# Optimization experiments

Hardware: AMD Instinct MI355X
Metric: run time of the kernel (lower is better)

## Reference

```python
import jax, jax.numpy as jnp
import numpy as np


def _fake_quant(x, bits, axis):
    """AQT-style abs-max symmetric fake quantization.

    IntNumerics(bits, preserve_zero=True, preserve_max_val=True, clip=True,
    round=True) with AbsMaxCalibration: bound = 2^(bits-1)-1,
    scale = absmax/bound (stop-gradient), q = round(clip(x/scale)),
    dequant = q*scale. Round uses straight-through estimator.
    """
    bound = float(2 ** (bits - 1) - 1)
    absmax = jax.lax.stop_gradient(
        jnp.max(jnp.abs(x), axis=axis, keepdims=True))
    scale = absmax / bound
    scale = jnp.where(scale == 0.0, jnp.ones_like(scale), scale)
    s = x / scale
    clipped = jnp.clip(s, -bound, bound)  # clip_gradient=True semantics
    rounded = clipped + jax.lax.stop_gradient(jnp.round(clipped) - clipped)
    return rounded * scale


def setup_inputs() -> dict:
    key = jax.random.key(0)
    k1, k2, k3 = jax.random.split(key, 3)
    B, S, D, F = 4, 2048, 4096, 4096
    x = jax.random.normal(k1, (B, S, D), dtype=jnp.float32)
    # lecun_normal over (in, out)
    kernel = jax.random.normal(k2, (D, F), dtype=jnp.float32) / np.sqrt(D)
    bias = jax.random.normal(k3, (F,), dtype=jnp.float32) * 0.01
    return {"x": x, "kernel": kernel, "bias": bias}


def reference(x, kernel, bias):
    # int8 fake-quant of activations: abs-max over contracting (last) axis
    xq = _fake_quant(x, bits=8, axis=-1)
    # int8 fake-quant of kernel: abs-max over contracting axis (0) -> per out-col
    kq = _fake_quant(kernel, bits=8, axis=0)
    # quantized dot_general: contract last axis of x with axis 0 of kernel
    y = jnp.einsum('bsd,df->bsf', xq, kq)
    # int16 fake-quant of bias (calibration_axes=-1 over the whole vector)
    bq16 = _fake_quant(bias, bits=16, axis=-1)
    y = y + bq16[None, None, :]
    # int8 output requant, per-row abs-max over feature axis
    out = _fake_quant(y, bits=8, axis=-1)
    return out
```

## Files before the change

### kernel.cpp

```cpp
#include <hip/hip_runtime.h>
#include <stdint.h>

typedef int int32x4 __attribute__((ext_vector_type(4)));

#define M_ROWS 8192
#define K_DIM  4096
#define N_DIM  4096

#define GPTR(p) ((const __attribute__((address_space(1))) unsigned int*)(p))
#define LPTR(p) ((__attribute__((address_space(3))) unsigned int*)(p))

__device__ __forceinline__ float block_absmax_256(float v, float* red) {
#pragma unroll
  for (int off = 32; off > 0; off >>= 1)
    v = fmaxf(v, __shfl_down(v, off, 64));
  const int w = threadIdx.x >> 6;
  if ((threadIdx.x & 63) == 0) red[w] = v;
  __syncthreads();
  return fmaxf(fmaxf(red[0], red[1]), fmaxf(red[2], red[3]));
}

__global__ void quant_x_kernel(const float* __restrict__ x,
                               int8_t* __restrict__ qx,
                               float* __restrict__ sx) {
  __shared__ float red[4];
  const int row = blockIdx.x;
  const int t = threadIdx.x;
  const float* xr = x + (size_t)row * K_DIM;
  float4 v[4];
  float m = 0.0f;
#pragma unroll
  for (int i = 0; i < 4; ++i) {
    v[i] = *(const float4*)(xr + t * 16 + i * 4);
    m = fmaxf(m, fmaxf(fmaxf(fabsf(v[i].x), fabsf(v[i].y)),
                       fmaxf(fabsf(v[i].z), fabsf(v[i].w))));
  }
  float amax = block_absmax_256(m, red);
  float scale = amax / 127.0f;
  if (scale == 0.0f) scale = 1.0f;
  if (t == 0) sx[row] = scale;
  int words[4];
#pragma unroll
  for (int i = 0; i < 4; ++i) {
    float a = fminf(fmaxf(v[i].x / scale, -127.0f), 127.0f);
    float b = fminf(fmaxf(v[i].y / scale, -127.0f), 127.0f);
    float c = fminf(fmaxf(v[i].z / scale, -127.0f), 127.0f);
    float d = fminf(fmaxf(v[i].w / scale, -127.0f), 127.0f);
    int qa = (int)rintf(a), qb = (int)rintf(b), qc = (int)rintf(c), qd = (int)rintf(d);
    words[i] = (qa & 255) | ((qb & 255) << 8) | ((qc & 255) << 16) | ((qd & 255) << 24);
  }
  *(int4*)(qx + (size_t)row * K_DIM + t * 16) =
      make_int4(words[0], words[1], words[2], words[3]);
}

__global__ void colmax_kernel(const float* __restrict__ k,
                              unsigned int* __restrict__ cm) {
  const int c = blockIdx.x * 256 + threadIdx.x;
  const int r0 = blockIdx.y * 128;
  float m = 0.0f;
  for (int i = 0; i < 128; ++i)
    m = fmaxf(m, fabsf(k[(size_t)(r0 + i) * N_DIM + c]));
  atomicMax(&cm[c], __float_as_uint(m));
}

__global__ void finalize_kernel(const float* __restrict__ cm,
                                float* __restrict__ sk,
                                const float* __restrict__ bias,
                                float* __restrict__ bq) {
  __shared__ float red[4];
  const int t = threadIdx.x;
  if (blockIdx.x < 16) {
    const int c = blockIdx.x * 256 + t;
    float s = cm[c] / 127.0f;
    if (s == 0.0f) s = 1.0f;
    sk[c] = s;
  } else {
    float4 v[4];
    float m = 0.0f;
#pragma unroll
    for (int i = 0; i < 4; ++i) {
      v[i] = *(const float4*)(bias + t * 16 + i * 4);
      m = fmaxf(m, fmaxf(fmaxf(fabsf(v[i].x), fabsf(v[i].y)),
                         fmaxf(fabsf(v[i].z), fabsf(v[i].w))));
    }
    float amax = block_absmax_256(m, red);
    float s = amax / 32767.0f;
    if (s == 0.0f) s = 1.0f;
#pragma unroll
    for (int i = 0; i < 4; ++i) {
      float4 o;
      o.x = rintf(fminf(fmaxf(v[i].x / s, -32767.0f), 32767.0f)) * s;
      o.y = rintf(fminf(fmaxf(v[i].y / s, -32767.0f), 32767.0f)) * s;
      o.z = rintf(fminf(fmaxf(v[i].z / s, -32767.0f), 32767.0f)) * s;
      o.w = rintf(fminf(fmaxf(v[i].w / s, -32767.0f), 32767.0f)) * s;
      *(float4*)(bq + t * 16 + i * 4) = o;
    }
  }
}

__global__ void quant_kT_kernel(const float* __restrict__ kern,
                                const float* __restrict__ cm,
                                int8_t* __restrict__ qkT) {
  __shared__ int8_t tile[64][68];
  const int t = threadIdx.x;
  const int c0 = blockIdx.x * 64;
  const int r0 = blockIdx.y * 64;
  const int tc = t & 63;
  const int tr = t >> 6;
  float s = cm[c0 + tc] / 127.0f;
  if (s == 0.0f) s = 1.0f;
#pragma unroll
  for (int i = 0; i < 16; ++i) {
    const int r = r0 + tr + i * 4;
    float u = kern[(size_t)r * N_DIM + c0 + tc] / s;
    u = fminf(fmaxf(u, -127.0f), 127.0f);
    tile[tc][tr + i * 4] = (int8_t)rintf(u);
  }
  __syncthreads();
  const int cl = t >> 2;
  const int ch = (t & 3) * 16;
  int w4[4];
#pragma unroll
  for (int j = 0; j < 4; ++j) w4[j] = *(const int*)&tile[cl][ch + j * 4];
  *(int4*)(qkT + (size_t)(c0 + cl) * K_DIM + r0 + ch) =
      make_int4(w4[0], w4[1], w4[2], w4[3]);
}

#define BM 128
#define BN 128
#define BK 64

__global__ void gemm_kernel(const int8_t* __restrict__ qx,
                            const int8_t* __restrict__ qkT,
                            const float* __restrict__ sx,
                            const float* __restrict__ sk,
                            const float* __restrict__ bq,
                            float* __restrict__ out) {
  __shared__ int32x4 AsV[512];
  __shared__ int32x4 BsV[512];
  char* As = (char*)AsV;
  char* Bs = (char*)BsV;

  const int t = threadIdx.x;
  const int w = t >> 6;
  const int l = t & 63;
  const int wm = w >> 1, wn = w & 1;
  const int rowBase = blockIdx.y * BM;
  const int colBase = blockIdx.x * BN;

  const int sw = (l & 3) ^ ((l >> 2) & 3) ^ (l >> 4);

  const int8_t* gA = qx  + (size_t)(rowBase + (l >> 2)) * K_DIM + sw * 16;
  const int8_t* gB = qkT + (size_t)(colBase + (l >> 2)) * K_DIM + sw * 16;

  int aoff[4], boff[4];
#pragma unroll
  for (int mt = 0; mt < 4; ++mt)
    aoff[mt] = (wm * 64 + mt * 16 + (l & 15)) * 64 + sw * 16;
#pragma unroll
  for (int nt = 0; nt < 4; ++nt)
    boff[nt] = (wn * 64 + nt * 16 + (l & 15)) * 64 + sw * 16;

  int32x4 zero = {0, 0, 0, 0};
  int32x4 acc[4][4];
#pragma unroll
  for (int mt = 0; mt < 4; ++mt)
#pragma unroll
    for (int nt = 0; nt < 4; ++nt) acc[mt][nt] = zero;

  for (int k0 = 0; k0 < K_DIM; k0 += BK) {
    __syncthreads();
#pragma unroll
    for (int j = 0; j < 2; ++j) {
      const int chunk = j * 4 + w;
      __builtin_amdgcn_global_load_lds(
          GPTR(gA + (size_t)chunk * 16 * K_DIM + k0),
          LPTR(As + chunk * 1024), 16, 0, 0);
      __builtin_amdgcn_global_load_lds(
          GPTR(gB + (size_t)chunk * 16 * K_DIM + k0),
          LPTR(Bs + chunk * 1024), 16, 0, 0);
    }
    __syncthreads();

    int32x4 af[4], bf[4];
#pragma unroll
    for (int mt = 0; mt < 4; ++mt) af[mt] = *(const int32x4*)(As + aoff[mt]);
#pragma unroll
    for (int nt = 0; nt < 4; ++nt) bf[nt] = *(const int32x4*)(Bs + boff[nt]);
#pragma unroll
    for (int mt = 0; mt < 4; ++mt)
#pragma unroll
      for (int nt = 0; nt < 4; ++nt)
        acc[mt][nt] = __builtin_amdgcn_mfma_i32_16x16x64_i8(
            af[mt], bf[nt], acc[mt][nt], 0, 0, 0);
  }

  const int lr = (l >> 4) * 4;
  const int lc = l & 15;
#pragma unroll
  for (int mt = 0; mt < 4; ++mt) {
    const int r0 = rowBase + wm * 64 + mt * 16 + lr;
    float sxr[4];
#pragma unroll
    for (int r = 0; r < 4; ++r) sxr[r] = sx[r0 + r];
#pragma unroll
    for (int nt = 0; nt < 4; ++nt) {
      const int c = colBase + wn * 64 + nt * 16 + lc;
      const float skc = sk[c];
      const float bqc = bq[c];
#pragma unroll
      for (int r = 0; r < 4; ++r)
        out[(size_t)(r0 + r) * N_DIM + c] =
            (float)acc[mt][nt][r] * (sxr[r] * skc) + bqc;
    }
  }
}

__global__ void requant_kernel(float* __restrict__ y) {
  __shared__ float red[4];
  const int row = blockIdx.x;
  const int t = threadIdx.x;
  float* yr = y + (size_t)row * N_DIM;
  float4 v[4];
  float m = 0.0f;
#pragma unroll
  for (int i = 0; i < 4; ++i) {
    v[i] = *(const float4*)(yr + i * 1024 + t * 4);
    m = fmaxf(m, fmaxf(fmaxf(fabsf(v[i].x), fabsf(v[i].y)),
                       fmaxf(fabsf(v[i].z), fabsf(v[i].w))));
  }
  float amax = block_absmax_256(m, red);
  float s = amax / 127.0f;
  if (s == 0.0f) s = 1.0f;
#pragma unroll
  for (int i = 0; i < 4; ++i) {
    float4 o;
    o.x = rintf(fminf(fmaxf(v[i].x / s, -127.0f), 127.0f)) * s;
    o.y = rintf(fminf(fmaxf(v[i].y / s, -127.0f), 127.0f)) * s;
    o.z = rintf(fminf(fmaxf(v[i].z / s, -127.0f), 127.0f)) * s;
    o.w = rintf(fminf(fmaxf(v[i].w / s, -127.0f), 127.0f)) * s;
    *(float4*)(yr + i * 1024 + t * 4) = o;
  }
}

extern "C" void kernel_launch(void* const* d_in, const int* in_sizes, int n_in,
                              void* d_out, int out_size, void* d_ws, size_t ws_size,
                              hipStream_t stream) {
  (void)in_sizes; (void)n_in; (void)out_size; (void)ws_size;
  const float* x    = (const float*)d_in[0];
  const float* kern = (const float*)d_in[1];
  const float* bias = (const float*)d_in[2];
  float* out = (float*)d_out;

  char* w8 = (char*)d_ws;
  int8_t* qx  = (int8_t*)w8;
  int8_t* qkT = (int8_t*)(w8 + 33554432);
  float* sx   = (float*)(w8 + 50331648);
  float* cm   = (float*)(w8 + 50331648 + 32768);
  float* sk   = (float*)(w8 + 50331648 + 49152);
  float* bq   = (float*)(w8 + 50331648 + 65536);

  hipMemsetAsync(cm, 0, 4096 * sizeof(float), stream);
  quant_x_kernel<<<M_ROWS, 256, 0, stream>>>(x, qx, sx);
  colmax_kernel<<<dim3(16, 32), 256, 0, stream>>>(kern, (unsigned int*)cm);
  finalize_kernel<<<17, 256, 0, stream>>>(cm, sk, bias, bq);
  quant_kT_kernel<<<dim3(64, 64), 256, 0, stream>>>(kern, cm, qkT);
  gemm_kernel<<<dim3(N_DIM / BN, M_ROWS / BM), 256, 0, stream>>>(qx, qkT, sx, sk, bq, out);
  requant_kernel<<<M_ROWS, 256, 0, stream>>>(out);
}
```

Baseline: 503.6 us.

## Double GEMM K-tile to 128 with new LDS swizzle and vectorize kernel quant

The GEMM K-step doubles from 64 to 128. Each iteration now loads twice as much A and B into LDS, using a new 8-row-per-chunk XOR swizzle, and runs two MFMA sub-steps. This halves the number of barrier pairs and loop iterations per output tile, at the cost of double the LDS use, which may reduce occupancy. The kernel-transpose quantizer now reads float4 vectors and writes int4 rows from a padded tile, cutting the number of global load instructions.

```diff
diff --git a/kernel.cpp b/kernel.cpp
--- a/kernel.cpp
+++ b/kernel.cpp
@@ -101,34 +101,37 @@
 __global__ void quant_kT_kernel(const float* __restrict__ kern,
                                 const float* __restrict__ cm,
                                 int8_t* __restrict__ qkT) {
-  __shared__ int8_t tile[64][68];
+  __shared__ int8_t tile[64][80];
   const int t = threadIdx.x;
   const int c0 = blockIdx.x * 64;
   const int r0 = blockIdx.y * 64;
-  const int tc = t & 63;
-  const int tr = t >> 6;
-  float s = cm[c0 + tc] / 127.0f;
-  if (s == 0.0f) s = 1.0f;
-#pragma unroll
-  for (int i = 0; i < 16; ++i) {
-    const int r = r0 + tr + i * 4;
-    float u = kern[(size_t)r * N_DIM + c0 + tc] / s;
-    u = fminf(fmaxf(u, -127.0f), 127.0f);
-    tile[tc][tr + i * 4] = (int8_t)rintf(u);
+  const int colg = (t & 15) * 4;
+  const int row = t >> 4;
+  float s[4];
+#pragma unroll
+  for (int j = 0; j < 4; ++j) {
+    float v = cm[c0 + colg + j] / 127.0f;
+    s[j] = (v == 0.0f) ? 1.0f : v;
+  }
+#pragma unroll
+  for (int i = 0; i < 4; ++i) {
+    const int r = row + i * 16;
+    float4 v = *(const float4*)&kern[(size_t)(r0 + r) * N_DIM + c0 + colg];
+    tile[colg + 0][r] = (int8_t)rintf(fminf(fmaxf(v.x / s[0], -127.0f), 127.0f));
+    tile[colg + 1][r] = (int8_t)rintf(fminf(fmaxf(v.y / s[1], -127.0f), 127.0f));
+    tile[colg + 2][r] = (int8_t)rintf(fminf(fmaxf(v.z / s[2], -127.0f), 127.0f));
+    tile[colg + 3][r] = (int8_t)rintf(fminf(fmaxf(v.w / s[3], -127.0f), 127.0f));
   }
   __syncthreads();
-  const int cl = t >> 2;
-  const int ch = (t & 3) * 16;
-  int w4[4];
-#pragma unroll
-  for (int j = 0; j < 4; ++j) w4[j] = *(const int*)&tile[cl][ch + j * 4];
-  *(int4*)(qkT + (size_t)(c0 + cl) * K_DIM + r0 + ch) =
-      make_int4(w4[0], w4[1], w4[2], w4[3]);
+  const int f = t >> 2;
+  const int seg = (t & 3) * 16;
+  int4 w = *(const int4*)&tile[f][seg];
+  *(int4*)(qkT + (size_t)(c0 + f) * K_DIM + r0 + seg) = w;
 }
 
 #define BM 128
 #define BN 128
-#define BK 64
+#define BK 128
 
 __global__ void gemm_kernel(const int8_t* __restrict__ qx,
                             const int8_t* __restrict__ qkT,
@@ -136,8 +139,8 @@
                             const float* __restrict__ sk,
                             const float* __restrict__ bq,
                             float* __restrict__ out) {
-  __shared__ int32x4 AsV[512];
-  __shared__ int32x4 BsV[512];
+  __shared__ int32x4 AsV[1024];
+  __shared__ int32x4 BsV[1024];
   char* As = (char*)AsV;
   char* Bs = (char*)BsV;
 
@@ -148,18 +151,21 @@
   const int rowBase = blockIdx.y * BM;
   const int colBase = blockIdx.x * BN;
 
-  const int sw = (l & 3) ^ ((l >> 2) & 3) ^ (l >> 4);
-
-  const int8_t* gA = qx  + (size_t)(rowBase + (l >> 2)) * K_DIM + sw * 16;
-  const int8_t* gB = qkT + (size_t)(colBase + (l >> 2)) * K_DIM + sw * 16;
-
-  int aoff[4], boff[4];
+  const int8_t* gA = qx  + (size_t)(rowBase + (l >> 3)) * K_DIM
+                         + (((l & 7) ^ (l >> 3)) * 16);
+  const int8_t* gB = qkT + (size_t)(colBase + (l >> 3)) * K_DIM
+                         + (((l & 7) ^ (l >> 3)) * 16);
+
+  int arow[4], brow[4], soff[2];
 #pragma unroll
   for (int mt = 0; mt < 4; ++mt)
-    aoff[mt] = (wm * 64 + mt * 16 + (l & 15)) * 64 + sw * 16;
+    arow[mt] = (wm * 64 + mt * 16 + (l & 15)) * 128;
 #pragma unroll
   for (int nt = 0; nt < 4; ++nt)
-    boff[nt] = (wn * 64 + nt * 16 + (l & 15)) * 64 + sw * 16;
+    brow[nt] = (wn * 64 + nt * 16 + (l & 15)) * 128;
+#pragma unroll
+  for (int s = 0; s < 2; ++s)
+    soff[s] = ((s * 4 + (l >> 4)) ^ (l & 7)) * 16;
 
   int32x4 zero = {0, 0, 0, 0};
   int32x4 acc[4][4];
@@ -171,28 +177,33 @@
   for (int k0 = 0; k0 < K_DIM; k0 += BK) {
     __syncthreads();
 #pragma unroll
-    for (int j = 0; j < 2; ++j) {
-      const int chunk = j * 4 + w;
+    for (int j = 0; j < 4; ++j) {
+      const int ca = j * 4 + w;
       __builtin_amdgcn_global_load_lds(
-          GPTR(gA + (size_t)chunk * 16 * K_DIM + k0),
-          LPTR(As + chunk * 1024), 16, 0, 0);
+          GPTR(gA + (size_t)ca * 8 * K_DIM + k0),
+          LPTR(As + ca * 1024), 16, 0, 0);
       __builtin_amdgcn_global_load_lds(
-          GPTR(gB + (size_t)chunk * 16 * K_DIM + k0),
-          LPTR(Bs + chunk * 1024), 16, 0, 0);
+          GPTR(gB + (size_t)ca * 8 * K_DIM + k0),
+          LPTR(Bs + ca * 1024), 16, 0, 0);
     }
     __syncthreads();
 
-    int32x4 af[4], bf[4];
-#pragma unroll
-    for (int mt = 0; mt < 4; ++mt) af[mt] = *(const int32x4*)(As + aoff[mt]);
-#pragma unroll
-    for (int nt = 0; nt < 4; ++nt) bf[nt] = *(const int32x4*)(Bs + boff[nt]);
-#pragma unroll
-    for (int mt = 0; mt < 4; ++mt)
+#pragma unroll
+    for (int s = 0; s < 2; ++s) {
+      int32x4 af[4], bf[4];
+#pragma unroll
+      for (int mt = 0; mt < 4; ++mt)
+        af[mt] = *(const int32x4*)(As + arow[mt] + soff[s]);
 #pragma unroll
       for (int nt = 0; nt < 4; ++nt)
-        acc[mt][nt] = __builtin_amdgcn_mfma_i32_16x16x64_i8(
-            af[mt], bf[nt], acc[mt][nt], 0, 0, 0);
+        bf[nt] = *(const int32x4*)(Bs + brow[nt] + soff[s]);
+#pragma unroll
+      for (int mt = 0; mt < 4; ++mt)
+#pragma unroll
+        for (int nt = 0; nt < 4; ++nt)
+          acc[mt][nt] = __builtin_amdgcn_mfma_i32_16x16x64_i8(
+              af[mt], bf[nt], acc[mt][nt], 0, 0, 0);
+    }
   }
 
   const int lr = (l >> 4) * 4;
```

Result: faster. 469.3 us (-6.8%).
